# Optimization experiments

Hardware: AMD Instinct MI355X
Metric: run time of the kernel (lower is better)

## Reference

```python
import jax, jax.numpy as jnp
import numpy as np

D = 32          # embedding_size
B = 16384       # batch_size
P = 16          # neighbor_sample_size (paths per item per hop)
NE = 100000     # n_entity
NU = 100000     # n_user
NR = 32         # n_relation
N_ITER = 2


def setup_inputs() -> dict:
    key = jax.random.key(0)
    ks = jax.random.split(key, 20)
    s = 0.1
    nrm = lambda k, sh: jax.random.normal(k, sh, dtype=jnp.float32) * s
    inp = {
        "user_table": nrm(ks[0], (NU, D)),
        "ent_table": nrm(ks[1], (NE, D)),
        "rel_table": nrm(ks[2], (NR, D)),
        # PyTorch LSTM params, gate order (i, f, g, o)
        "w_ih0": nrm(ks[3], (4 * D, 2 * D)),
        "w_hh0": nrm(ks[4], (4 * D, D)),
        "b_ih0": nrm(ks[5], (4 * D,)),
        "b_hh0": nrm(ks[6], (4 * D,)),
        "w_ih1": nrm(ks[7], (4 * D, 2 * D)),
        "w_hh1": nrm(ks[8], (4 * D, D)),
        "b_ih1": nrm(ks[9], (4 * D,)),
        "b_hh1": nrm(ks[10], (4 * D,)),
        "agg_w": nrm(ks[11], (D, D)),
        "agg_b": nrm(ks[12], (D,)),
        "users": jax.random.randint(ks[13], (B,), 0, NU),
        "items": jax.random.randint(ks[14], (B,), 0, NE),
        "ratings": jax.random.randint(ks[15], (B,), 0, 2),
        # hop h path table: [n_entity, P, 2*(h+1)+1]; values < 32 valid for both tables
        "lp0": jax.random.randint(ks[16], (NE, P, 3), 0, 32),
        "lp1": jax.random.randint(ks[17], (NE, P, 5), 0, 32),
    }
    return inp


def _lstm_last(seq, w_ih, w_hh, b_ih, b_hh):
    # seq: [N, T, 2D] -> final hidden state [N, D], PyTorch gate order i,f,g,o
    N = seq.shape[0]
    H = w_hh.shape[1]
    bias = b_ih + b_hh

    def step(carry, x):
        h, c = carry
        g = x @ w_ih.T + h @ w_hh.T + bias
        i, f, gg, o = jnp.split(g, 4, axis=-1)
        c = jax.nn.sigmoid(f) * c + jax.nn.sigmoid(i) * jnp.tanh(gg)
        h = jax.nn.sigmoid(o) * jnp.tanh(c)
        return (h, c), None

    h0 = jnp.zeros((N, H), seq.dtype)
    (h, _), _ = jax.lax.scan(step, (h0, h0), jnp.swapaxes(seq, 0, 1))
    return h


def _forward(user_table, ent_table, rel_table, lstm_params, agg_w, agg_b,
             users, items, ratings, lps):
    u = user_table[users]                # [B, D]
    items_emb = ent_table[items]         # [B, D]
    for hop in range(N_ITER):
        lp = lps[hop]
        w_ih, w_hh, b_ih, b_hh = lstm_params[hop]
        il = lp[items]                   # [B, P, 2*(hop+1)+1]
        seed_e = ent_table[il[:, :, 0]]  # [B, P, D]
        u_b = jnp.broadcast_to(u[:, None, :], seed_e.shape)
        first = jnp.concatenate([u_b, seed_e], -1)[:, :, None, :]   # [B,P,1,2D]
        rel_e = rel_table[il[:, :, 1::2]]                            # [B,P,hop+1,D]
        tail_e = ent_table[il[:, :, 2::2]]                           # [B,P,hop+1,D]
        rest = jnp.concatenate([rel_e, tail_e], -1)                  # [B,P,hop+1,2D]
        seq = jnp.concatenate([first, rest], 2).reshape(B * P, hop + 2, 2 * D)
        h = _lstm_last(seq, w_ih, w_hh, b_ih, b_hh)                  # [B*P, D]
        final = h.reshape(B, P, D).sum(axis=1)                       # hidden_out sum
        items_emb = (items_emb + final) @ agg_w.T + agg_b            # 'sum' aggregator
    scores = jnp.sum(u * items_emb, axis=-1)                         # [B]
    r = ratings.astype(scores.dtype)
    # stable BCE on sigmoid(scores)
    loss = -jnp.mean(r * jax.nn.log_sigmoid(scores) + (1.0 - r) * jax.nn.log_sigmoid(-scores))
    return loss, jax.nn.sigmoid(scores)


def reference(user_table, ent_table, rel_table,
              w_ih0, w_hh0, b_ih0, b_hh0,
              w_ih1, w_hh1, b_ih1, b_hh1,
              agg_w, agg_b,
              users, items, ratings, lp0, lp1):
    lstm_params = [(w_ih0, w_hh0, b_ih0, b_hh0), (w_ih1, w_hh1, b_ih1, b_hh1)]
    loss, scores_normalized = _forward(user_table, ent_table, rel_table,
                                       lstm_params, agg_w, agg_b,
                                       users, items, ratings, (lp0, lp1))
    return (loss, scores_normalized, items)
```

## Files before the change

### kernel.cpp

```cpp
#include <hip/hip_runtime.h>
#include <math.h>

#define D  32
#define BN 16384
#define PP 16

typedef __bf16 bf16x8 __attribute__((ext_vector_type(8)));
typedef __bf16 bf16x4 __attribute__((ext_vector_type(4)));
typedef float  floatx4 __attribute__((ext_vector_type(4)));

#define K1 1.44269504088896341f
#define K2 2.88539008177792681f

#define WU_OFF     0
#define WHH_OFF    10240
#define WIMG_BYTES 20480
#define H_OFF      20480
#define LDS_BYTES  (WIMG_BYTES + 8 * 1280)

__device__ __forceinline__ float sigf(float x) {
    float e = __builtin_amdgcn_exp2f(-x * K1);
    return __builtin_amdgcn_rcpf(1.0f + e);
}
__device__ __forceinline__ float logsigf(float x) {
    float ax = fabsf(x);
    float l = log1pf(__expf(-ax));
    return (x >= 0.0f) ? -l : x - l;
}
__device__ __forceinline__ bf16x8 loadu8(const float* __restrict__ p) {
    float4 a = ((const float4*)p)[0], b = ((const float4*)p)[1];
    bf16x8 r = { (__bf16)a.x, (__bf16)a.y, (__bf16)a.z, (__bf16)a.w,
                 (__bf16)b.x, (__bf16)b.y, (__bf16)b.z, (__bf16)b.w };
    return r;
}

__global__ __launch_bounds__(256)
void prep_tables(const float* __restrict__ ent, const float* __restrict__ rel,
                 const float* __restrict__ wih0, const float* __restrict__ whh0,
                 const float* __restrict__ bih0, const float* __restrict__ bhh0,
                 const float* __restrict__ wih1, const float* __restrict__ whh1,
                 const float* __restrict__ bih1, const float* __restrict__ bhh1,
                 float* __restrict__ T0, float* __restrict__ T,
                 float* __restrict__ wimg)
{
    const int id = blockIdx.x * 256 + threadIdx.x;
    if (id < 16384) {
        const int hop  = id >> 13;
        const int rest = id & 8191;
        const int mat  = rest >> 12;
        const int e    = rest & 4095;
        const int gate = e >> 5, d = e & 31;
        float v = mat ? (hop ? whh1 : whh0)[(size_t)gate * 32 + d]
                      : (hop ? wih1 : wih0)[(size_t)gate * 64 + d];
        __bf16* base = (__bf16*)((char*)wimg + hop * WIMG_BYTES + mat * 10240);
        base[gate * 40 + d] = (__bf16)v;
    } else if (id < 16384 + 262144) {
        const int idt = id - 16384;
        const int hop = idt >> 17;
        const int r   = idt & 131071;
        const int j   = r >> 12;
        const int k   = (r >> 7) & 31;
        const int g   = r & 127;
        const float* wih = hop ? wih1 : wih0;
        const float4* w4 = (const float4*)(wih + (size_t)g * 64);
        const float4* r4 = (const float4*)(rel + (size_t)j * 32);
        const float4* e4 = (const float4*)(ent + (size_t)k * 32);
        float a = hop ? bih1[g] + bhh1[g] : bih0[g] + bhh0[g];
        #pragma unroll
        for (int i = 0; i < 8; ++i) {
            float4 w = w4[i], x = r4[i];
            a = fmaf(w.x, x.x, a); a = fmaf(w.y, x.y, a);
            a = fmaf(w.z, x.z, a); a = fmaf(w.w, x.w, a);
        }
        #pragma unroll
        for (int i = 0; i < 8; ++i) {
            float4 w = w4[8 + i], x = e4[i];
            a = fmaf(w.x, x.x, a); a = fmaf(w.y, x.y, a);
            a = fmaf(w.z, x.z, a); a = fmaf(w.w, x.w, a);
        }
        T[(size_t)hop * 131072 + r] = a;
    } else if (id < 16384 + 262144 + 8192) {
        const int idb = id - 16384 - 262144;
        const int hop = idb >> 12;
        const int k   = (idb >> 7) & 31;
        const int g   = idb & 127;
        const float* wih = hop ? wih1 : wih0;
        const float4* w4 = (const float4*)(wih + (size_t)g * 64);
        const float4* e4 = (const float4*)(ent + (size_t)k * 32);
        float a = hop ? bih1[g] + bhh1[g] : bih0[g] + bhh0[g];
        #pragma unroll
        for (int i = 0; i < 8; ++i) {
            float4 w = w4[8 + i], x = e4[i];
            a = fmaf(w.x, x.x, a); a = fmaf(w.y, x.y, a);
            a = fmaf(w.z, x.z, a); a = fmaf(w.w, x.w, a);
        }
        T0[(size_t)hop * 4096 + k * 128 + g] = a;
    }
}

template<bool FIRST, bool LAST>
__device__ __forceinline__ void nonlin(
    floatx4* __restrict__ acc, float* __restrict__ cst,
    float* __restrict__ hlo, float* __restrict__ hhi,
    char* __restrict__ Hw, int q, int bnl)
{
    #pragma unroll
    for (int hf = 0; hf < 2; ++hf) {
        float* hout = hf ? hhi : hlo;
        #pragma unroll
        for (int r = 0; r < 4; ++r) {
            float gi = acc[0 + hf][r], gf = acc[2 + hf][r],
                  gg = acc[4 + hf][r], go = acc[6 + hf][r];
            float Ai = 1.0f + __builtin_amdgcn_exp2f(-gi * K1);
            float Af = 1.0f + __builtin_amdgcn_exp2f(-gf * K1);
            float G2 = __builtin_amdgcn_exp2f(gg * K2);
            float Gp = G2 + 1.0f, Gm = G2 - 1.0f;
            float cold = FIRST ? 0.0f : cst[hf * 4 + r];
            float num = cold * Ai * Gp + Gm * Af;
            float c = num * __builtin_amdgcn_rcpf(Af * Ai * Gp);
            cst[hf * 4 + r] = c;
            float Ao = 1.0f + __builtin_amdgcn_exp2f(-go * K1);
            float C2 = __builtin_amdgcn_exp2f(c * K2);
            hout[r] = (C2 - 1.0f) * __builtin_amdgcn_rcpf(Ao * (C2 + 1.0f));
        }
    }
    if (!LAST) {
        bf16x4 plo = { (__bf16)hlo[0], (__bf16)hlo[1], (__bf16)hlo[2], (__bf16)hlo[3] };
        bf16x4 phi = { (__bf16)hhi[0], (__bf16)hhi[1], (__bf16)hhi[2], (__bf16)hhi[3] };
        *(bf16x4*)(Hw + bnl * 80 + 8 * q)      = plo;
        *(bf16x4*)(Hw + bnl * 80 + 32 + 8 * q) = phi;
    }
}

__global__ __launch_bounds__(256, 3)
void hop_mfma(const float* __restrict__ user_table,
              const int*   __restrict__ users,
              const int*   __restrict__ items,
              const int*   __restrict__ lp0,
              const int*   __restrict__ lp1,
              const float* __restrict__ wimg,
              const float* __restrict__ T0g,
              const float* __restrict__ Tg,
              float* __restrict__ F0,
              float* __restrict__ F1)
{
    __shared__ __align__(16) char lds[LDS_BYTES];

    const bool second = blockIdx.x & 1;
    const int  idx    = blockIdx.x >> 1;
    const int tid  = threadIdx.x;
    const int lane = tid & 63;
    const int wave = tid >> 6;
    const int q    = lane >> 4;
    const int bnl  = lane & 15;

    {
        const float4* g4 = (const float4*)((const char*)wimg +
                                           (second ? WIMG_BYTES : 0));
        float4* l4 = (float4*)lds;
        #pragma unroll
        for (int i = 0; i < 5; ++i) l4[i * 256 + tid] = g4[i * 256 + tid];
    }

    const char* Wu  = lds + WU_OFF;
    const char* Whh = lds + WHH_OFF;
    char* HwA = lds + H_OFF + (wave * 2 + 0) * 1280;
    char* HwB = lds + H_OFF + (wave * 2 + 1) * 1280;

    const int fbA = idx * 8 + wave;
    const int fbB = fbA + 4;
    const int L   = second ? 5 : 3;
    const int* lp = second ? lp1 : lp0;
    const int* __restrict__ ilA = lp + ((size_t)items[fbA] * PP + bnl) * L;
    const int* __restrict__ ilB = lp + ((size_t)items[fbB] * PP + bnl) * L;
    int sqA[5], sqB[5];
    #pragma unroll
    for (int i = 0; i < 5; ++i) {
        sqA[i] = (i < L) ? ilA[i] : 0;
        sqB[i] = (i < L) ? ilB[i] : 0;
    }

    bf16x8 buA = loadu8(user_table + (size_t)users[fbA] * D + q * 8);
    bf16x8 buB = loadu8(user_table + (size_t)users[fbB] * D + q * 8);

    const float* T0h = T0g + (second ? 4096 : 0);
    const float* Th  = Tg  + (second ? 131072 : 0);

    __syncthreads();

    float cstA[8], cstB[8], hloA[4], hhiA[4], hloB[4], hhiB[4];

    {
        const float* tA = T0h + sqA[0] * 128 + 4 * q;
        const float* tB = T0h + sqB[0] * 128 + 4 * q;
        floatx4 accA[8], accB[8];
        #pragma unroll
        for (int mt = 0; mt < 8; ++mt) {
            accA[mt] = *(const floatx4*)(tA + 16 * mt);
            accB[mt] = *(const floatx4*)(tB + 16 * mt);
        }
        #pragma unroll
        for (int mt = 0; mt < 8; ++mt) {
            bf16x8 wu = *(const bf16x8*)(Wu + (16 * mt + bnl) * 80 + q * 16);
            accA[mt] = __builtin_amdgcn_mfma_f32_16x16x32_bf16(wu, buA, accA[mt], 0, 0, 0);
            accB[mt] = __builtin_amdgcn_mfma_f32_16x16x32_bf16(wu, buB, accB[mt], 0, 0, 0);
        }
        nonlin<true, false>(accA, cstA, hloA, hhiA, HwA, q, bnl);
        nonlin<true, false>(accB, cstB, hloB, hhiB, HwB, q, bnl);
    }

    #pragma unroll
    for (int t = 1; t < 3; ++t) {
        if (t == 2 && !second) break;
        const bool last = (t == (second ? 2 : 1));
        const float* tA = Th + (((sqA[2 * t - 1]) << 5) + sqA[2 * t]) * 128 + 4 * q;
        const float* tB = Th + (((sqB[2 * t - 1]) << 5) + sqB[2 * t]) * 128 + 4 * q;
        floatx4 accA[8], accB[8];
        #pragma unroll
        for (int mt = 0; mt < 8; ++mt) {
            accA[mt] = *(const floatx4*)(tA + 16 * mt);
            accB[mt] = *(const floatx4*)(tB + 16 * mt);
        }
        bf16x8 bhA = *(const bf16x8*)(HwA + bnl * 80 + q * 16);
        bf16x8 bhB = *(const bf16x8*)(HwB + bnl * 80 + q * 16);
        #pragma unroll
        for (int mt = 0; mt < 8; ++mt) {
            bf16x8 wh = *(const bf16x8*)(Whh + (16 * mt + bnl) * 80 + q * 16);
            accA[mt] = __builtin_amdgcn_mfma_f32_16x16x32_bf16(wh, bhA, accA[mt], 0, 0, 0);
            accB[mt] = __builtin_amdgcn_mfma_f32_16x16x32_bf16(wh, bhB, accB[mt], 0, 0, 0);
        }
        if (last) {
            nonlin<false, true>(accA, cstA, hloA, hhiA, HwA, q, bnl);
            nonlin<false, true>(accB, cstB, hloB, hhiB, HwB, q, bnl);
        } else {
            nonlin<false, false>(accA, cstA, hloA, hhiA, HwA, q, bnl);
            nonlin<false, false>(accB, cstB, hloB, hhiB, HwB, q, bnl);
        }
    }

    #pragma unroll
    for (int r = 0; r < 4; ++r) {
        #pragma unroll
        for (int m = 1; m < 16; m <<= 1) {
            hloA[r] += __shfl_xor(hloA[r], m);
            hhiA[r] += __shfl_xor(hhiA[r], m);
            hloB[r] += __shfl_xor(hloB[r], m);
            hhiB[r] += __shfl_xor(hhiB[r], m);
        }
    }
    if (bnl == 0) {
        float* Fout = (second ? F1 : F0);
        float4 vloA = { hloA[0], hloA[1], hloA[2], hloA[3] };
        float4 vhiA = { hhiA[0], hhiA[1], hhiA[2], hhiA[3] };
        float4 vloB = { hloB[0], hloB[1], hloB[2], hloB[3] };
        float4 vhiB = { hhiB[0], hhiB[1], hhiB[2], hhiB[3] };
        *(float4*)(Fout + (size_t)fbA * D + 4 * q)      = vloA;
        *(float4*)(Fout + (size_t)fbA * D + 16 + 4 * q) = vhiA;
        *(float4*)(Fout + (size_t)fbB * D + 4 * q)      = vloB;
        *(float4*)(Fout + (size_t)fbB * D + 16 + 4 * q) = vhiB;
    }
}

__global__ __launch_bounds__(256)
void chain_score(const float* __restrict__ user_table,
                 const float* __restrict__ ent_table,
                 const float* __restrict__ agg_w,
                 const float* __restrict__ agg_b,
                 const int*   __restrict__ users,
                 const int*   __restrict__ items,
                 const int*   __restrict__ ratings,
                 const float* __restrict__ F0,
                 const float* __restrict__ F1,
                 float* __restrict__ out,
                 float* __restrict__ partials)
{
    __shared__ float s[8][33];
    __shared__ float red[8];
    const int tid = threadIdx.x;
    const int bb  = tid >> 5;
    const int j   = tid & 31;
    const int b   = blockIdx.x * 8 + bb;
    const int it  = items[b];

    s[bb][j] = ent_table[(size_t)it * D + j] + F0[(size_t)b * D + j];
    __syncthreads();
    const float* __restrict__ w = agg_w + (size_t)j * D;
    float e0 = agg_b[j];
    #pragma unroll
    for (int k = 0; k < D; ++k) e0 = fmaf(s[bb][k], w[k], e0);
    __syncthreads();
    s[bb][j] = e0 + F1[(size_t)b * D + j];
    __syncthreads();
    float e1 = agg_b[j];
    #pragma unroll
    for (int k = 0; k < D; ++k) e1 = fmaf(s[bb][k], w[k], e1);

    float prod = user_table[(size_t)users[b] * D + j] * e1;
    #pragma unroll
    for (int m = 1; m < 32; m <<= 1) prod += __shfl_xor(prod, m);
    if (j == 0) {
        out[1 + b]      = sigf(prod);
        out[1 + BN + b] = (float)it;
        float r = (float)ratings[b];
        red[bb] = r * logsigf(prod) + (1.0f - r) * logsigf(-prod);
    }
    __syncthreads();
    if (tid == 0) {
        float t = 0.0f;
        #pragma unroll
        for (int qq = 0; qq < 8; ++qq) t += red[qq];
        partials[blockIdx.x] = t;
    }
}

__global__ __launch_bounds__(256)
void loss_kernel(const float* __restrict__ partials, float* __restrict__ out)
{
    __shared__ float red[4];
    const int t = threadIdx.x;
    float v = 0.0f;
    #pragma unroll
    for (int qq = 0; qq < 8; ++qq) v += partials[qq * 256 + t];
    #pragma unroll
    for (int m = 1; m < 64; m <<= 1) v += __shfl_xor(v, m);
    if ((t & 63) == 0) red[t >> 6] = v;
    __syncthreads();
    if (t == 0) out[0] = -(red[0] + red[1] + red[2] + red[3]) / (float)BN;
}

extern "C" void kernel_launch(void* const* d_in, const int* in_sizes, int n_in,
                              void* d_out, int out_size, void* d_ws, size_t ws_size,
                              hipStream_t stream)
{
    const float* user_table = (const float*)d_in[0];
    const float* ent_table  = (const float*)d_in[1];
    const float* rel_table  = (const float*)d_in[2];
    const float* w_ih0 = (const float*)d_in[3];
    const float* w_hh0 = (const float*)d_in[4];
    const float* b_ih0 = (const float*)d_in[5];
    const float* b_hh0 = (const float*)d_in[6];
    const float* w_ih1 = (const float*)d_in[7];
    const float* w_hh1 = (const float*)d_in[8];
    const float* b_ih1 = (const float*)d_in[9];
    const float* b_hh1 = (const float*)d_in[10];
    const float* agg_w = (const float*)d_in[11];
    const float* agg_b = (const float*)d_in[12];
    const int* users   = (const int*)d_in[13];
    const int* items   = (const int*)d_in[14];
    const int* ratings = (const int*)d_in[15];
    const int* lp0     = (const int*)d_in[16];
    const int* lp1     = (const int*)d_in[17];
    float* out = (float*)d_out;

    float* ws       = (float*)d_ws;
    float* F0       = ws;
    float* F1       = F0 + (size_t)BN * D;
    float* partials = F1 + (size_t)BN * D;
    float* T0       = partials + 2048;
    float* T        = T0 + 8192;
    float* wimg     = T + 262144;

    prep_tables<<<1120, 256, 0, stream>>>(ent_table, rel_table,
        w_ih0, w_hh0, b_ih0, b_hh0, w_ih1, w_hh1, b_ih1, b_hh1, T0, T, wimg);
    hop_mfma<<<4096, 256, 0, stream>>>(
        user_table, users, items, lp0, lp1, wimg, T0, T, F0, F1);
    chain_score<<<BN / 8, 256, 0, stream>>>(
        user_table, ent_table, agg_w, agg_b, users, items, ratings,
        F0, F1, out, partials);
    loss_kernel<<<1, 256, 0, stream>>>(partials, out);
}
```

Baseline: 270.2 us.

## Process one batch row per wave and prefetch all gate tables early

Result: no change. 272.4 us (+0.8%).

```diff
diff --git a/kernel.cpp b/kernel.cpp
--- a/kernel.cpp
+++ b/kernel.cpp
@@ -16,7 +16,7 @@
 #define WHH_OFF    10240
 #define WIMG_BYTES 20480
 #define H_OFF      20480
-#define LDS_BYTES  (WIMG_BYTES + 8 * 1280)
+#define LDS_BYTES  (WIMG_BYTES + 4 * 1280)
 
 __device__ __forceinline__ float sigf(float x) {
     float e = __builtin_amdgcn_exp2f(-x * K1);
@@ -132,7 +132,7 @@
     }
 }
 
-__global__ __launch_bounds__(256, 3)
+__global__ __launch_bounds__(256, 4)
 void hop_mfma(const float* __restrict__ user_table,
               const int*   __restrict__ users,
               const int*   __restrict__ items,
@@ -154,6 +154,27 @@
     const int q    = lane >> 4;
     const int bnl  = lane & 15;
 
+    const int fb = idx * 4 + wave;
+    const int L  = second ? 5 : 3;
+    const int* lp = second ? lp1 : lp0;
+    const int* __restrict__ il = lp + ((size_t)items[fb] * PP + bnl) * L;
+    int sq[5];
+    #pragma unroll
+    for (int i = 0; i < 5; ++i) sq[i] = (i < L) ? il[i] : 0;
+
+    const float* T0h = T0g + (second ? 4096 : 0);
+    const float* Th  = Tg  + (second ? 131072 : 0);
+    const float* t0p = T0h + sq[0] * 128 + 4 * q;
+    const float* t1p = Th + (((sq[1]) << 5) + sq[2]) * 128 + 4 * q;
+
+    floatx4 acc0[8], acc1[8];
+    #pragma unroll
+    for (int mt = 0; mt < 8; ++mt) acc0[mt] = *(const floatx4*)(t0p + 16 * mt);
+    #pragma unroll
+    for (int mt = 0; mt < 8; ++mt) acc1[mt] = *(const floatx4*)(t1p + 16 * mt);
+
+    bf16x8 bu = loadu8(user_table + (size_t)users[fb] * D + q * 8);
+
     {
         const float4* g4 = (const float4*)((const char*)wimg +
                                            (second ? WIMG_BYTES : 0));
@@ -161,103 +182,63 @@
         #pragma unroll
         for (int i = 0; i < 5; ++i) l4[i * 256 + tid] = g4[i * 256 + tid];
     }
-
     const char* Wu  = lds + WU_OFF;
     const char* Whh = lds + WHH_OFF;
-    char* HwA = lds + H_OFF + (wave * 2 + 0) * 1280;
-    char* HwB = lds + H_OFF + (wave * 2 + 1) * 1280;
-
-    const int fbA = idx * 8 + wave;
-    const int fbB = fbA + 4;
-    const int L   = second ? 5 : 3;
-    const int* lp = second ? lp1 : lp0;
-    const int* __restrict__ ilA = lp + ((size_t)items[fbA] * PP + bnl) * L;
-    const int* __restrict__ ilB = lp + ((size_t)items[fbB] * PP + bnl) * L;
-    int sqA[5], sqB[5];
-    #pragma unroll
-    for (int i = 0; i < 5; ++i) {
-        sqA[i] = (i < L) ? ilA[i] : 0;
-        sqB[i] = (i < L) ? ilB[i] : 0;
-    }
-
-    bf16x8 buA = loadu8(user_table + (size_t)users[fbA] * D + q * 8);
-    bf16x8 buB = loadu8(user_table + (size_t)users[fbB] * D + q * 8);
-
-    const float* T0h = T0g + (second ? 4096 : 0);
-    const float* Th  = Tg  + (second ? 131072 : 0);
-
-    __syncthreads();
-
-    float cstA[8], cstB[8], hloA[4], hhiA[4], hloB[4], hhiB[4];
+    char* Hw = lds + H_OFF + wave * 1280;
+
+    __syncthreads();
+
+    float cst[8], hlo[4], hhi[4];
+
+    #pragma unroll
+    for (int mt = 0; mt < 8; ++mt) {
+        bf16x8 wu = *(const bf16x8*)(Wu + (16 * mt + bnl) * 80 + q * 16);
+        acc0[mt] = __builtin_amdgcn_mfma_f32_16x16x32_bf16(wu, bu, acc0[mt], 0, 0, 0);
+    }
+    nonlin<true, false>(acc0, cst, hlo, hhi, Hw, q, bnl);
+
+    floatx4 acc2[8];
+    if (second) {
+        const float* t2p = Th + (((sq[3]) << 5) + sq[4]) * 128 + 4 * q;
+        #pragma unroll
+        for (int mt = 0; mt < 8; ++mt) acc2[mt] = *(const floatx4*)(t2p + 16 * mt);
+    }
 
     {
-        const float* tA = T0h + sqA[0] * 128 + 4 * q;
-        const float* tB = T0h + sqB[0] * 128 + 4 * q;
-        floatx4 accA[8], accB[8];
-        #pragma unroll
-        for (int mt = 0; mt < 8; ++mt) {
-            accA[mt] = *(const floatx4*)(tA + 16 * mt);
-            accB[mt] = *(const floatx4*)(tB + 16 * mt);
-        }
-        #pragma unroll
-        for (int mt = 0; mt < 8; ++mt) {
-            bf16x8 wu = *(const bf16x8*)(Wu + (16 * mt + bnl) * 80 + q * 16);
-            accA[mt] = __builtin_amdgcn_mfma_f32_16x16x32_bf16(wu, buA, accA[mt], 0, 0, 0);
-            accB[mt] = __builtin_amdgcn_mfma_f32_16x16x32_bf16(wu, buB, accB[mt], 0, 0, 0);
-        }
-        nonlin<true, false>(accA, cstA, hloA, hhiA, HwA, q, bnl);
-        nonlin<true, false>(accB, cstB, hloB, hhiB, HwB, q, bnl);
-    }
-
-    #pragma unroll
-    for (int t = 1; t < 3; ++t) {
-        if (t == 2 && !second) break;
-        const bool last = (t == (second ? 2 : 1));
-        const float* tA = Th + (((sqA[2 * t - 1]) << 5) + sqA[2 * t]) * 128 + 4 * q;
-        const float* tB = Th + (((sqB[2 * t - 1]) << 5) + sqB[2 * t]) * 128 + 4 * q;
-        floatx4 accA[8], accB[8];
-        #pragma unroll
-        for (int mt = 0; mt < 8; ++mt) {
-            accA[mt] = *(const floatx4*)(tA + 16 * mt);
-            accB[mt] = *(const floatx4*)(tB + 16 * mt);
-        }
-        bf16x8 bhA = *(const bf16x8*)(HwA + bnl * 80 + q * 16);
-        bf16x8 bhB = *(const bf16x8*)(HwB + bnl * 80 + q * 16);
+        bf16x8 bh = *(const bf16x8*)(Hw + bnl * 80 + q * 16);
         #pragma unroll
         for (int mt = 0; mt < 8; ++mt) {
             bf16x8 wh = *(const bf16x8*)(Whh + (16 * mt + bnl) * 80 + q * 16);
-            accA[mt] = __builtin_amdgcn_mfma_f32_16x16x32_bf16(wh, bhA, accA[mt], 0, 0, 0);
-            accB[mt] = __builtin_amdgcn_mfma_f32_16x16x32_bf16(wh, bhB, accB[mt], 0, 0, 0);
-        }
-        if (last) {
-            nonlin<false, true>(accA, cstA, hloA, hhiA, HwA, q, bnl);
-            nonlin<false, true>(accB, cstB, hloB, hhiB, HwB, q, bnl);
-        } else {
-            nonlin<false, false>(accA, cstA, hloA, hhiA, HwA, q, bnl);
-            nonlin<false, false>(accB, cstB, hloB, hhiB, HwB, q, bnl);
-        }
+            acc1[mt] = __builtin_amdgcn_mfma_f32_16x16x32_bf16(wh, bh, acc1[mt], 0, 0, 0);
+        }
+        if (second) nonlin<false, false>(acc1, cst, hlo, hhi, Hw, q, bnl);
+        else        nonlin<false, true >(acc1, cst, hlo, hhi, Hw, q, bnl);
+    }
+
+    if (second) {
+        bf16x8 bh = *(const bf16x8*)(Hw + bnl * 80 + q * 16);
+        #pragma unroll
+        for (int mt = 0; mt < 8; ++mt) {
+            bf16x8 wh = *(const bf16x8*)(Whh + (16 * mt + bnl) * 80 + q * 16);
+            acc2[mt] = __builtin_amdgcn_mfma_f32_16x16x32_bf16(wh, bh, acc2[mt], 0, 0, 0);
+        }
+        nonlin<false, true>(acc2, cst, hlo, hhi, Hw, q, bnl);
     }
 
     #pragma unroll
     for (int r = 0; r < 4; ++r) {
         #pragma unroll
         for (int m = 1; m < 16; m <<= 1) {
-            hloA[r] += __shfl_xor(hloA[r], m);
-            hhiA[r] += __shfl_xor(hhiA[r], m);
-            hloB[r] += __shfl_xor(hloB[r], m);
-            hhiB[r] += __shfl_xor(hhiB[r], m);
+            hlo[r] += __shfl_xor(hlo[r], m);
+            hhi[r] += __shfl_xor(hhi[r], m);
         }
     }
     if (bnl == 0) {
         float* Fout = (second ? F1 : F0);
-        float4 vloA = { hloA[0], hloA[1], hloA[2], hloA[3] };
-        float4 vhiA = { hhiA[0], hhiA[1], hhiA[2], hhiA[3] };
-        float4 vloB = { hloB[0], hloB[1], hloB[2], hloB[3] };
-        float4 vhiB = { hhiB[0], hhiB[1], hhiB[2], hhiB[3] };
-        *(float4*)(Fout + (size_t)fbA * D + 4 * q)      = vloA;
-        *(float4*)(Fout + (size_t)fbA * D + 16 + 4 * q) = vhiA;
-        *(float4*)(Fout + (size_t)fbB * D + 4 * q)      = vloB;
-        *(float4*)(Fout + (size_t)fbB * D + 16 + 4 * q) = vhiB;
+        float4 vlo = { hlo[0], hlo[1], hlo[2], hlo[3] };
+        float4 vhi = { hhi[0], hhi[1], hhi[2], hhi[3] };
+        *(float4*)(Fout + (size_t)fb * D + 4 * q)      = vlo;
+        *(float4*)(Fout + (size_t)fb * D + 16 + 4 * q) = vhi;
     }
 }
 
@@ -362,7 +343,7 @@
 
     prep_tables<<<1120, 256, 0, stream>>>(ent_table, rel_table,
         w_ih0, w_hh0, b_ih0, b_hh0, w_ih1, w_hh1, b_ih1, b_hh1, T0, T, wimg);
-    hop_mfma<<<4096, 256, 0, stream>>>(
+    hop_mfma<<<8192, 256, 0, stream>>>(
         user_table, users, items, lp0, lp1, wimg, T0, T, F0, F1);
     chain_score<<<BN / 8, 256, 0, stream>>>(
         user_table, ent_table, agg_w, agg_b, users, items, ratings,
```
